# Kernel optimization log

Hardware: AMD Instinct MI355X
Metric: run time of the kernel (lower is better)

## Reference

```python
import jax, jax.numpy as jnp
import numpy as np

N, F, E, LIN, C, B = 16384, 500, 128, 128, 10, 4096
P_EDGE = 0.002  # ~32 avg degree


def _l2norm(x):
    # F.normalize(dim=1), eps=1e-12
    n = jnp.linalg.norm(x, axis=1, keepdims=True)
    return x / jnp.maximum(n, 1e-12)


def setup_inputs() -> dict:
    key = jax.random.key(0)
    ks = jax.random.split(key, 10)
    adj = (jax.random.uniform(ks[0], (N, N)) < P_EDGE).astype(jnp.float32)
    idx = jnp.arange(N)
    adj = adj.at[idx, idx].set(1.0)  # self-loops guarantee degree >= 1
    data = jax.random.normal(ks[1], (N, F), dtype=jnp.float32)
    nodes = jax.random.randint(ks[2], (B,), 0, N)
    # Encoder 1: Linear(2F -> E); Encoder 2: Linear(2E -> E); classifier heads
    W1 = jax.random.normal(ks[3], (E, 2 * F), dtype=jnp.float32) * 0.03
    b1 = jnp.zeros((E,), jnp.float32)
    W2 = jax.random.normal(ks[4], (E, 2 * E), dtype=jnp.float32) * 0.06
    b2 = jnp.zeros((E,), jnp.float32)
    Wl1 = jax.random.normal(ks[5], (LIN, E), dtype=jnp.float32) * 0.08
    bl1 = jnp.zeros((LIN,), jnp.float32)
    Wl2 = jax.random.normal(ks[6], (C, LIN), dtype=jnp.float32) * 0.12
    bl2 = jnp.zeros((C,), jnp.float32)
    return {"nodes": nodes, "adj": adj, "data": data,
            "W1": W1, "b1": b1, "W2": W2, "b2": b2,
            "Wl1": Wl1, "bl1": bl1, "Wl2": Wl2, "bl2": bl2}


def reference(nodes, adj, data, W1, b1, W2, b2, Wl1, bl1, Wl2, bl2):
    deg = jnp.sum(adj, axis=1, keepdims=True)  # [N,1]
    # Layer 1 (mean aggregator over full neighbor set): computed for all nodes
    neigh1 = (adj @ data) / deg                               # [N,F]
    h1 = jnp.concatenate([data, neigh1], axis=1)              # [N,2F] (self, neigh)
    H1 = _l2norm(jax.nn.relu(h1 @ W1.T + b1))                 # [N,E]
    # Layer 2: only for the queried node batch
    neigh2 = (adj[nodes] @ H1) / deg[nodes]                   # [B,E]
    h2 = jnp.concatenate([H1[nodes], neigh2], axis=1)         # [B,2E]
    H2 = _l2norm(jax.nn.relu(h2 @ W2.T + b2))                 # [B,E]
    x = H2 @ Wl1.T + bl1                                      # [B,LIN]
    x = x @ Wl2.T + bl2                                       # [B,C]
    return jax.nn.softmax(x, axis=1)
```

## Files before the change

### kernel.cpp

```cpp
#include <hip/hip_runtime.h>
#include <math.h>
#include <stddef.h>

#define N_NODES 16384
#define F_DIM   500
#define E_DIM   128
#define C_DIM   10
#define B_DIM   4096
#define MAXDEG  128

typedef __attribute__((ext_vector_type(8))) short short8;
typedef __attribute__((ext_vector_type(4))) float f32x4;

__device__ inline unsigned short f2bf(float f) {
    union { float f; unsigned int u; } v; v.f = f;
    unsigned int u = v.u;
    u += 0x7FFFu + ((u >> 16) & 1u);
    return (unsigned short)(u >> 16);
}
__device__ inline float bf2f(unsigned short u) {
    union { unsigned int u; float f; } v; v.u = (unsigned int)u << 16;
    return v.f;
}

__global__ __launch_bounds__(256) void k_front(const float* __restrict__ adj,
                                               const float* __restrict__ data,
                                               const float* __restrict__ W1,
                                               const float* __restrict__ W2,
                                               const float* __restrict__ Wl1,
                                               unsigned short* __restrict__ nbr,
                                               int* __restrict__ deg,
                                               unsigned short* __restrict__ Xb16,
                                               unsigned short* __restrict__ W2ab16,
                                               unsigned short* __restrict__ W2bb16,
                                               float* __restrict__ Wl1t) {
    const int bb = blockIdx.x;
    const int tid = threadIdx.x;

    if (bb < 4096) {
        const int lane = tid & 63;
        const int row = bb * 4 + (tid >> 6);
        const float4* r4 = (const float4*)(adj + (size_t)row * N_NODES);
        const size_t nb = (size_t)row * MAXDEG;
        const unsigned long long lowm = ~0ull >> (64 - lane - 1) >> 1;
        int base = 0;
#define PROC1(val, cix) do {                                                  \
        bool p = (val) != 0.f;                                                \
        unsigned long long m = __ballot(p);                                   \
        if (p) {                                                              \
            int pos = base + (int)__popcll(m & lowm);                         \
            if (pos < MAXDEG) nbr[nb + pos] = (unsigned short)(cix);          \
        }                                                                     \
        base += (int)__popcll(m);                                             \
    } while (0)
#define PROC4(vv, tt) do {                                                    \
        int colb = ((tt) * 64 + lane) * 4;                                    \
        PROC1((vv).x, colb);                                                  \
        PROC1((vv).y, colb + 1);                                              \
        PROC1((vv).z, colb + 2);                                              \
        PROC1((vv).w, colb + 3);                                              \
    } while (0)
        float4 cur = r4[lane];
#pragma unroll 4
        for (int t = 0; t < 63; ++t) {
            float4 nxt = r4[(t + 1) * 64 + lane];
            PROC4(cur, t);
            cur = nxt;
        }
        PROC4(cur, 63);
#undef PROC4
#undef PROC1
        if (lane == 0) deg[row] = (base > MAXDEG) ? MAXDEG : base;
        return;
    } else if (bb < 4160) {
        int idx = (bb - 4096) * 256 + tid;
        int n = idx >> 7, k = idx & 127;
        W2ab16[idx] = f2bf(W2[(size_t)n * 256 + k]);
        return;
    } else if (bb < 4224) {
        int idx = (bb - 4160) * 256 + tid;
        int n = idx >> 7, k = idx & 127;
        W2bb16[idx] = f2bf(W2[(size_t)n * 256 + 128 + k]);
        return;
    } else if (bb < 4240) {
        __shared__ float tile[32][33];
        int tb = bb - 4224;
        int k0 = (tb & 3) * 32, e0 = (tb >> 2) * 32;
        int tx = tid & 31, ty0 = tid >> 5;
#pragma unroll
        for (int q = 0; q < 4; ++q) {
            int ty = ty0 + q * 8;
            tile[ty][tx] = Wl1[(size_t)(e0 + ty) * 128 + k0 + tx];
        }
        __syncthreads();
#pragma unroll
        for (int q = 0; q < 4; ++q) {
            int ty = ty0 + q * 8;
            Wl1t[(size_t)(k0 + ty) * 128 + e0 + tx] = tile[tx][ty];
        }
        return;
    }
    __shared__ unsigned short sA[32 * 40];
    __shared__ unsigned short sB[256 * 40];
    const int g = bb - 4240;
    const int blockM = g * 32;
    const int w    = tid >> 6;
    const int lane = tid & 63;
    const int l16  = lane & 15;
    const int quad = lane >> 4;
    f32x4 acc[2][4] = {};
#pragma unroll 1
    for (int c = 0; c < 16; ++c) {
        const int k0 = c << 5;
        {
            int row = tid >> 3, ch = tid & 7;
            int k = k0 + ch * 4;
            const float* p = data + (size_t)(blockM + row) * F_DIM + k;
            float4 f = (k + 4 <= F_DIM) ? *(const float4*)p
                                        : make_float4(0.f, 0.f, 0.f, 0.f);
            ushort4 u;
            u.x = f2bf(f.x); u.y = f2bf(f.y); u.z = f2bf(f.z); u.w = f2bf(f.w);
            *(ushort4*)(sA + row * 40 + ch * 4) = u;
        }
#pragma unroll
        for (int q = 0; q < 8; ++q) {
            int idx = tid + 256 * q;
            int row = idx >> 3, ch = idx & 7;
            int k = k0 + ch * 4;
            const float* p = W1 + (size_t)(row & 127) * 1000 + (row >> 7) * F_DIM + k;
            float4 f = (k + 4 <= F_DIM) ? *(const float4*)p
                                        : make_float4(0.f, 0.f, 0.f, 0.f);
            ushort4 u;
            u.x = f2bf(f.x); u.y = f2bf(f.y); u.z = f2bf(f.z); u.w = f2bf(f.w);
            *(ushort4*)(sB + row * 40 + ch * 4) = u;
        }
        __syncthreads();
        short8 af[2], bfr[4];
#pragma unroll
        for (int mt = 0; mt < 2; ++mt)
            af[mt] = *(const short8*)(sA + (mt * 16 + l16) * 40 + quad * 8);
#pragma unroll
        for (int nt = 0; nt < 4; ++nt)
            bfr[nt] = *(const short8*)(sB + (w * 64 + nt * 16 + l16) * 40 + quad * 8);
#pragma unroll
        for (int mt = 0; mt < 2; ++mt)
#pragma unroll
            for (int nt = 0; nt < 4; ++nt)
                acc[mt][nt] = __builtin_amdgcn_mfma_f32_16x16x32_bf16(af[mt], bfr[nt], acc[mt][nt], 0, 0, 0);
        __syncthreads();
    }
#pragma unroll
    for (int mt = 0; mt < 2; ++mt)
#pragma unroll
        for (int nt = 0; nt < 4; ++nt) {
            int col = w * 64 + nt * 16 + l16;
#pragma unroll
            for (int r = 0; r < 4; ++r) {
                int row = blockM + mt * 16 + quad * 4 + r;
                Xb16[(size_t)row * 256 + col] = f2bf(acc[mt][nt][r]);
            }
        }
}

__global__ __launch_bounds__(256) void k_gather(const unsigned short* __restrict__ nbr,
                                                const int* __restrict__ deg,
                                                const unsigned short* __restrict__ Xb16,
                                                const float* __restrict__ b1,
                                                unsigned short* __restrict__ H1b) {
    const int i = blockIdx.x;
    const int t = threadIdx.x;
    const int cnt = deg[i];
    __shared__ int s_idx[MAXDEG];
    __shared__ float s_part[8][128];
    __shared__ float s_w[2];
    if (t < cnt) s_idx[t] = nbr[(size_t)i * MAXDEG + t];
    __syncthreads();
    const int g = t >> 5, l = t & 31;
    float4 a4 = make_float4(0.f, 0.f, 0.f, 0.f);
    for (int k = g; k < cnt; k += 8) {
        ushort4 x4 = ((const ushort4*)(Xb16 + (size_t)s_idx[k] * 256 + 128))[l];
        a4.x += bf2f(x4.x); a4.y += bf2f(x4.y); a4.z += bf2f(x4.z); a4.w += bf2f(x4.w);
    }
    *(float4*)&s_part[g][l * 4] = a4;
    __syncthreads();
    float vv = 0.f;
    if (t < 128) {
        float tot = 0.f;
#pragma unroll
        for (int g2 = 0; g2 < 8; ++g2) tot += s_part[g2][t];
        vv = bf2f(Xb16[(size_t)i * 256 + t]) + tot / (float)cnt + b1[t];
        vv = fmaxf(vv, 0.f);
        float s = vv * vv;
#pragma unroll
        for (int off = 32; off > 0; off >>= 1) s += __shfl_down(s, off, 64);
        if ((t & 63) == 0) s_w[t >> 6] = s;
    }
    __syncthreads();
    if (t < 128) {
        float denom = fmaxf(sqrtf(s_w[0] + s_w[1]), 1e-12f);
        H1b[(size_t)i * 128 + t] = f2bf(vv / denom);
    }
}

__global__ __launch_bounds__(256) void k_gemm2(const unsigned short* __restrict__ H1b,
                                               const unsigned short* __restrict__ W2bb16,
                                               const unsigned short* __restrict__ W2ab16,
                                               const int* __restrict__ nodes,
                                               unsigned short* __restrict__ Yb16,
                                               float* __restrict__ Ya) {
    const int bb = blockIdx.x;
    const bool selfp = (bb >= 512);
    const unsigned short* B = selfp ? W2ab16 : W2bb16;
    const int blockM = (selfp ? (bb - 512) : bb) * 32;
    const int tid  = threadIdx.x;
    const int w    = tid >> 6;
    const int lane = tid & 63;
    const int l16  = lane & 15;
    const int quad = lane >> 4;
    int rsrc0 = blockM + l16,      rsrc1 = blockM + 16 + l16;
    if (selfp) { rsrc0 = nodes[rsrc0]; rsrc1 = nodes[rsrc1]; }
    short8 af[2][4], bfr[2][4];
#pragma unroll
    for (int c = 0; c < 4; ++c) {
        af[0][c] = *(const short8*)(H1b + (size_t)rsrc0 * 128 + c * 32 + quad * 8);
        af[1][c] = *(const short8*)(H1b + (size_t)rsrc1 * 128 + c * 32 + quad * 8);
    }
#pragma unroll
    for (int nt = 0; nt < 2; ++nt) {
        int n = w * 32 + nt * 16 + l16;
#pragma unroll
        for (int c = 0; c < 4; ++c)
            bfr[nt][c] = *(const short8*)(B + (size_t)n * 128 + c * 32 + quad * 8);
    }
    f32x4 acc[2][2] = {};
#pragma unroll
    for (int c = 0; c < 4; ++c)
#pragma unroll
        for (int mt = 0; mt < 2; ++mt)
#pragma unroll
            for (int nt = 0; nt < 2; ++nt)
                acc[mt][nt] = __builtin_amdgcn_mfma_f32_16x16x32_bf16(af[mt][c], bfr[nt][c], acc[mt][nt], 0, 0, 0);
#pragma unroll
    for (int mt = 0; mt < 2; ++mt)
#pragma unroll
        for (int nt = 0; nt < 2; ++nt) {
            int col = w * 32 + nt * 16 + l16;
#pragma unroll
            for (int r = 0; r < 4; ++r) {
                int row = blockM + mt * 16 + quad * 4 + r;
                if (selfp) Ya[(size_t)row * 128 + col] = acc[mt][nt][r];
                else       Yb16[(size_t)row * 128 + col] = f2bf(acc[mt][nt][r]);
            }
        }
}

__global__ __launch_bounds__(256) void k_l2head(const int* __restrict__ nodes,
                                                const unsigned short* __restrict__ nbr,
                                                const int* __restrict__ deg,
                                                const unsigned short* __restrict__ Yb16,
                                                const float* __restrict__ Ya,
                                                const float* __restrict__ b2,
                                                const float* __restrict__ Wl1t,
                                                const float* __restrict__ bl1,
                                                const float* __restrict__ Wl2,
                                                const float* __restrict__ bl2,
                                                float* __restrict__ out) {
    const int lane = threadIdx.x & 63;
    const int b = blockIdx.x * 4 + (threadIdx.x >> 6);
    const int n = nodes[b];
    const int cnt = deg[n];
    const int myn  = (lane < cnt)      ? (int)nbr[(size_t)n * MAXDEG + lane]      : 0;
    const int myn2 = (lane + 64 < cnt) ? (int)nbr[(size_t)n * MAXDEG + lane + 64] : 0;
    const int half = lane >> 5, l32 = lane & 31;
    float ax = 0.f, ay = 0.f, az = 0.f, aw = 0.f;
    for (int k = half; k < cnt; k += 2) {
        int kk = k & 63;
        int j1 = __shfl(myn, kk);
        int j2 = __shfl(myn2, kk);
        int j = (k < 64) ? j1 : j2;
        ushort4 y4 = *(const ushort4*)(Yb16 + (size_t)j * 128 + l32 * 4);
        ax += bf2f(y4.x); ay += bf2f(y4.y); az += bf2f(y4.z); aw += bf2f(y4.w);
    }
    ax += __shfl_xor(ax, 32); ay += __shfl_xor(ay, 32);
    az += __shfl_xor(az, 32); aw += __shfl_xor(aw, 32);
    float4 ya = *(const float4*)(Ya + (size_t)b * 128 + l32 * 4);
    float4 bb = *(const float4*)(b2 + l32 * 4);
    float fc = (float)cnt;
    float h0 = fmaxf(ya.x + ax / fc + bb.x, 0.f);
    float h1 = fmaxf(ya.y + ay / fc + bb.y, 0.f);
    float h2 = fmaxf(ya.z + az / fc + bb.z, 0.f);
    float h3 = fmaxf(ya.w + aw / fc + bb.w, 0.f);
    float s = h0 * h0 + h1 * h1 + h2 * h2 + h3 * h3;
#pragma unroll
    for (int off = 16; off > 0; off >>= 1) s += __shfl_xor(s, off);
    float rden = 1.0f / fmaxf(sqrtf(s), 1e-12f);
    h0 *= rden; h1 *= rden; h2 *= rden; h3 *= rden;
    float2 bl = *(const float2*)(bl1 + 2 * lane);
    float x0 = bl.x, x1 = bl.y;
    const float* wl = Wl1t + 2 * lane;
    for (int m = 0; m < 32; ++m) {
        float k0 = __shfl(h0, m), k1 = __shfl(h1, m), k2 = __shfl(h2, m), k3 = __shfl(h3, m);
        float2 w0 = *(const float2*)(wl + (size_t)(m * 4 + 0) * 128);
        float2 w1 = *(const float2*)(wl + (size_t)(m * 4 + 1) * 128);
        float2 w2 = *(const float2*)(wl + (size_t)(m * 4 + 2) * 128);
        float2 w3 = *(const float2*)(wl + (size_t)(m * 4 + 3) * 128);
        x0 += k0 * w0.x + k1 * w1.x + k2 * w2.x + k3 * w3.x;
        x1 += k0 * w0.y + k1 * w1.y + k2 * w2.y + k3 * w3.y;
    }
    float cv[C_DIM];
#pragma unroll
    for (int cc = 0; cc < C_DIM; ++cc) {
        float2 w = *(const float2*)(Wl2 + (size_t)cc * 128 + 2 * lane);
        float p = x0 * w.x + x1 * w.y;
#pragma unroll
        for (int off = 32; off > 0; off >>= 1) p += __shfl_xor(p, off);
        cv[cc] = p + bl2[cc];
    }
    float mx = cv[0];
#pragma unroll
    for (int cc = 1; cc < C_DIM; ++cc) mx = fmaxf(mx, cv[cc]);
    float se = 0.f;
#pragma unroll
    for (int cc = 0; cc < C_DIM; ++cc) { cv[cc] = expf(cv[cc] - mx); se += cv[cc]; }
    float rse = 1.0f / se;
    float o = cv[0];
#pragma unroll
    for (int cc = 1; cc < C_DIM; ++cc) o = (lane == cc) ? cv[cc] : o;
    if (lane < C_DIM) out[(size_t)b * C_DIM + lane] = o * rse;
}

extern "C" void kernel_launch(void* const* d_in, const int* in_sizes, int n_in,
                              void* d_out, int out_size, void* d_ws, size_t ws_size,
                              hipStream_t stream) {
    const int*   nodes = (const int*)  d_in[0];
    const float* adj   = (const float*)d_in[1];
    const float* data  = (const float*)d_in[2];
    const float* W1    = (const float*)d_in[3];
    const float* b1    = (const float*)d_in[4];
    const float* W2    = (const float*)d_in[5];
    const float* b2    = (const float*)d_in[6];
    const float* Wl1   = (const float*)d_in[7];
    const float* bl1   = (const float*)d_in[8];
    const float* Wl2   = (const float*)d_in[9];
    const float* bl2   = (const float*)d_in[10];
    float* out = (float*)d_out;

    float* Wl1t = (float*)d_ws;
    float* Ya   = Wl1t + 16384;
    unsigned short* W2ab16 = (unsigned short*)(Ya + (size_t)B_DIM * 128);
    unsigned short* W2bb16 = W2ab16 + 16384;
    unsigned short* Xb16   = W2bb16 + 16384;
    unsigned short* H1b    = Xb16 + (size_t)N_NODES * 256;
    unsigned short* Yb16   = H1b + (size_t)N_NODES * 128;
    unsigned short* nbr    = Yb16 + (size_t)N_NODES * 128;
    int* deg = (int*)(nbr + (size_t)N_NODES * MAXDEG);

    k_front<<<4096 + 144 + 512, 256, 0, stream>>>(adj, data, W1, W2, Wl1,
                                                  nbr, deg, Xb16,
                                                  W2ab16, W2bb16, Wl1t);
    k_gather<<<N_NODES, 256, 0, stream>>>(nbr, deg, Xb16, b1, H1b);
    k_gemm2<<<512 + 128, 256, 0, stream>>>(H1b, W2bb16, W2ab16, nodes, Yb16, Ya);
    k_l2head<<<B_DIM / 4, 256, 0, stream>>>(nodes, nbr, deg, Yb16, Ya, b2,
                                            Wl1t, bl1, Wl2, bl2, out);
}
```

Measured before the change: 1.461 ms.

## Fuse adjacency scan with layer-1 neighbor aggregation and split weight prep kernel

The adjacency-row scan that built neighbor lists is moved out of the front kernel and fused with the layer-1 mean aggregation. Each wave now gathers the neighbor feature rows of Xb16 while it scans, then applies bias, ReLU and L2 normalisation in place. This removes the separate gather kernel, one launch and the round trip of neighbor lists through memory. The scan now depends on the prep GEMM output, so it must run after it, and the 1GB adjacency read is serialised behind the GEMM. Degree is no longer clamped, so the head kernel clamps the neighbor count itself; the adjacency read also gains deeper prefetch.

```diff
diff --git a/kernel.cpp b/kernel.cpp
--- a/kernel.cpp
+++ b/kernel.cpp
@@ -23,13 +23,10 @@
     return v.f;
 }
 
-__global__ __launch_bounds__(256) void k_front(const float* __restrict__ adj,
-                                               const float* __restrict__ data,
+__global__ __launch_bounds__(256) void k_prep1(const float* __restrict__ data,
                                                const float* __restrict__ W1,
                                                const float* __restrict__ W2,
                                                const float* __restrict__ Wl1,
-                                               unsigned short* __restrict__ nbr,
-                                               int* __restrict__ deg,
                                                unsigned short* __restrict__ Xb16,
                                                unsigned short* __restrict__ W2ab16,
                                                unsigned short* __restrict__ W2bb16,
@@ -37,54 +34,19 @@
     const int bb = blockIdx.x;
     const int tid = threadIdx.x;
 
-    if (bb < 4096) {
-        const int lane = tid & 63;
-        const int row = bb * 4 + (tid >> 6);
-        const float4* r4 = (const float4*)(adj + (size_t)row * N_NODES);
-        const size_t nb = (size_t)row * MAXDEG;
-        const unsigned long long lowm = ~0ull >> (64 - lane - 1) >> 1;
-        int base = 0;
-#define PROC1(val, cix) do {                                                  \
-        bool p = (val) != 0.f;                                                \
-        unsigned long long m = __ballot(p);                                   \
-        if (p) {                                                              \
-            int pos = base + (int)__popcll(m & lowm);                         \
-            if (pos < MAXDEG) nbr[nb + pos] = (unsigned short)(cix);          \
-        }                                                                     \
-        base += (int)__popcll(m);                                             \
-    } while (0)
-#define PROC4(vv, tt) do {                                                    \
-        int colb = ((tt) * 64 + lane) * 4;                                    \
-        PROC1((vv).x, colb);                                                  \
-        PROC1((vv).y, colb + 1);                                              \
-        PROC1((vv).z, colb + 2);                                              \
-        PROC1((vv).w, colb + 3);                                              \
-    } while (0)
-        float4 cur = r4[lane];
-#pragma unroll 4
-        for (int t = 0; t < 63; ++t) {
-            float4 nxt = r4[(t + 1) * 64 + lane];
-            PROC4(cur, t);
-            cur = nxt;
-        }
-        PROC4(cur, 63);
-#undef PROC4
-#undef PROC1
-        if (lane == 0) deg[row] = (base > MAXDEG) ? MAXDEG : base;
-        return;
-    } else if (bb < 4160) {
-        int idx = (bb - 4096) * 256 + tid;
+    if (bb < 64) {
+        int idx = bb * 256 + tid;
         int n = idx >> 7, k = idx & 127;
         W2ab16[idx] = f2bf(W2[(size_t)n * 256 + k]);
         return;
-    } else if (bb < 4224) {
-        int idx = (bb - 4160) * 256 + tid;
+    } else if (bb < 128) {
+        int idx = (bb - 64) * 256 + tid;
         int n = idx >> 7, k = idx & 127;
         W2bb16[idx] = f2bf(W2[(size_t)n * 256 + 128 + k]);
         return;
-    } else if (bb < 4240) {
+    } else if (bb < 144) {
         __shared__ float tile[32][33];
-        int tb = bb - 4224;
+        int tb = bb - 128;
         int k0 = (tb & 3) * 32, e0 = (tb >> 2) * 32;
         int tx = tid & 31, ty0 = tid >> 5;
 #pragma unroll
@@ -102,7 +64,7 @@
     }
     __shared__ unsigned short sA[32 * 40];
     __shared__ unsigned short sB[256 * 40];
-    const int g = bb - 4240;
+    const int g = bb - 144;
     const int blockM = g * 32;
     const int w    = tid >> 6;
     const int lane = tid & 63;
@@ -162,44 +124,54 @@
         }
 }
 
-__global__ __launch_bounds__(256) void k_gather(const unsigned short* __restrict__ nbr,
-                                                const int* __restrict__ deg,
-                                                const unsigned short* __restrict__ Xb16,
-                                                const float* __restrict__ b1,
-                                                unsigned short* __restrict__ H1b) {
-    const int i = blockIdx.x;
-    const int t = threadIdx.x;
-    const int cnt = deg[i];
-    __shared__ int s_idx[MAXDEG];
-    __shared__ float s_part[8][128];
-    __shared__ float s_w[2];
-    if (t < cnt) s_idx[t] = nbr[(size_t)i * MAXDEG + t];
-    __syncthreads();
-    const int g = t >> 5, l = t & 31;
-    float4 a4 = make_float4(0.f, 0.f, 0.f, 0.f);
-    for (int k = g; k < cnt; k += 8) {
-        ushort4 x4 = ((const ushort4*)(Xb16 + (size_t)s_idx[k] * 256 + 128))[l];
-        a4.x += bf2f(x4.x); a4.y += bf2f(x4.y); a4.z += bf2f(x4.z); a4.w += bf2f(x4.w);
-    }
-    *(float4*)&s_part[g][l * 4] = a4;
-    __syncthreads();
-    float vv = 0.f;
-    if (t < 128) {
-        float tot = 0.f;
-#pragma unroll
-        for (int g2 = 0; g2 < 8; ++g2) tot += s_part[g2][t];
-        vv = bf2f(Xb16[(size_t)i * 256 + t]) + tot / (float)cnt + b1[t];
-        vv = fmaxf(vv, 0.f);
-        float s = vv * vv;
-#pragma unroll
-        for (int off = 32; off > 0; off >>= 1) s += __shfl_down(s, off, 64);
-        if ((t & 63) == 0) s_w[t >> 6] = s;
-    }
-    __syncthreads();
-    if (t < 128) {
-        float denom = fmaxf(sqrtf(s_w[0] + s_w[1]), 1e-12f);
-        H1b[(size_t)i * 128 + t] = f2bf(vv / denom);
-    }
+__global__ __launch_bounds__(256) void k_scanagg(const float* __restrict__ adj,
+                                                 const unsigned short* __restrict__ Xb16,
+                                                 const float* __restrict__ b1,
+                                                 unsigned short* __restrict__ nbr,
+                                                 int* __restrict__ deg,
+                                                 unsigned short* __restrict__ H1b) {
+    const int lane = threadIdx.x & 63;
+    const int row = blockIdx.x * 4 + (threadIdx.x >> 6);
+    const float4* r4 = (const float4*)(adj + (size_t)row * N_NODES);
+    const size_t nb = (size_t)row * MAXDEG;
+    int base = 0;
+    float a0 = 0.f, a1 = 0.f;
+    float4 cur = r4[lane];
+    float4 nxt = r4[64 + lane];
+#pragma unroll 2
+    for (int t = 0; t < 64; ++t) {
+        int pf = (t + 2 < 64) ? (t + 2) : 63;
+        float4 nn2 = r4[pf * 64 + lane];
+#pragma unroll
+        for (int c = 0; c < 4; ++c) {
+            float val = (c == 0) ? cur.x : (c == 1) ? cur.y : (c == 2) ? cur.z : cur.w;
+            unsigned long long m = __ballot(val != 0.f);
+            while (m) {
+                int b = (int)__builtin_ctzll(m);
+                m &= m - 1;
+                int j = ((t * 64 + b) << 2) + c;
+                unsigned int u = ((const unsigned int*)(Xb16 + (size_t)j * 256 + 128))[lane];
+                a0 += bf2f((unsigned short)(u & 0xffffu));
+                a1 += bf2f((unsigned short)(u >> 16));
+                if (lane == 0 && base < MAXDEG) nbr[nb + base] = (unsigned short)j;
+                ++base;
+            }
+        }
+        cur = nxt;
+        nxt = nn2;
+    }
+    if (lane == 0) deg[row] = base;
+    unsigned int su = ((const unsigned int*)(Xb16 + (size_t)row * 256))[lane];
+    float2 bb = *(const float2*)(b1 + 2 * lane);
+    float fc = (float)base;
+    float v0 = fmaxf(bf2f((unsigned short)(su & 0xffffu)) + a0 / fc + bb.x, 0.f);
+    float v1 = fmaxf(bf2f((unsigned short)(su >> 16))     + a1 / fc + bb.y, 0.f);
+    float s = v0 * v0 + v1 * v1;
+#pragma unroll
+    for (int off = 32; off > 0; off >>= 1) s += __shfl_xor(s, off);
+    float rden = 1.0f / fmaxf(sqrtf(s), 1e-12f);
+    unsigned int o = (unsigned int)f2bf(v0 * rden) | ((unsigned int)f2bf(v1 * rden) << 16);
+    ((unsigned int*)(H1b + (size_t)row * 128))[lane] = o;
 }
 
 __global__ __launch_bounds__(256) void k_gemm2(const unsigned short* __restrict__ H1b,
@@ -269,11 +241,12 @@
     const int b = blockIdx.x * 4 + (threadIdx.x >> 6);
     const int n = nodes[b];
     const int cnt = deg[n];
-    const int myn  = (lane < cnt)      ? (int)nbr[(size_t)n * MAXDEG + lane]      : 0;
-    const int myn2 = (lane + 64 < cnt) ? (int)nbr[(size_t)n * MAXDEG + lane + 64] : 0;
+    const int gcnt = (cnt > MAXDEG) ? MAXDEG : cnt;
+    const int myn  = (lane < gcnt)      ? (int)nbr[(size_t)n * MAXDEG + lane]      : 0;
+    const int myn2 = (lane + 64 < gcnt) ? (int)nbr[(size_t)n * MAXDEG + lane + 64] : 0;
     const int half = lane >> 5, l32 = lane & 31;
     float ax = 0.f, ay = 0.f, az = 0.f, aw = 0.f;
-    for (int k = half; k < cnt; k += 2) {
+    for (int k = half; k < gcnt; k += 2) {
         int kk = k & 63;
         int j1 = __shfl(myn, kk);
         int j2 = __shfl(myn2, kk);
@@ -355,10 +328,9 @@
     unsigned short* nbr    = Yb16 + (size_t)N_NODES * 128;
     int* deg = (int*)(nbr + (size_t)N_NODES * MAXDEG);
 
-    k_front<<<4096 + 144 + 512, 256, 0, stream>>>(adj, data, W1, W2, Wl1,
-                                                  nbr, deg, Xb16,
-                                                  W2ab16, W2bb16, Wl1t);
-    k_gather<<<N_NODES, 256, 0, stream>>>(nbr, deg, Xb16, b1, H1b);
+    k_prep1<<<656, 256, 0, stream>>>(data, W1, W2, Wl1,
+                                     Xb16, W2ab16, W2bb16, Wl1t);
+    k_scanagg<<<N_NODES / 4, 256, 0, stream>>>(adj, Xb16, b1, nbr, deg, H1b);
     k_gemm2<<<512 + 128, 256, 0, stream>>>(H1b, W2bb16, W2ab16, nodes, Yb16, Ya);
     k_l2head<<<B_DIM / 4, 256, 0, stream>>>(nodes, nbr, deg, Yb16, Ya, b2,
                                             Wl1t, bl1, Wl2, bl2, out);
```

New measurement: 1.455 ms. Within noise of the previous version (-0.4%).
